# Performance work log

Hardware: AMD Instinct MI355X
Metric: run time of the kernel (lower is better)

## Reference

```python
import jax, jax.numpy as jnp
import numpy as np

B, C, N = 8, 512, 4096
G = 8          # GroupNorm groups (8 <= C)
EPS = 1e-6


def setup_inputs() -> dict:
    key = jax.random.key(0)
    ks = jax.random.split(key, 5)
    return {
        "x": jax.random.normal(ks[0], (B, C, N), dtype=jnp.float32),
        "qkv_w": jax.random.normal(ks[1], (3 * C, C), dtype=jnp.float32) * (C ** -0.5),
        "qkv_b": jax.random.normal(ks[2], (3 * C,), dtype=jnp.float32) * 0.02,
        "proj_w": jax.random.normal(ks[3], (C, C), dtype=jnp.float32) * (C ** -0.5),
        "proj_b": jax.random.normal(ks[4], (C,), dtype=jnp.float32) * 0.02,
        "gn_scale": jnp.ones((C,), dtype=jnp.float32),
        "gn_bias": jnp.zeros((C,), dtype=jnp.float32),
    }


def group_norm(x, scale, bias):
    b, c, n = x.shape
    xr = x.reshape(b, G, c // G, n)
    mean = xr.mean(axis=(2, 3), keepdims=True)
    var = xr.var(axis=(2, 3), keepdims=True)
    h = ((xr - mean) * jax.lax.rsqrt(var + EPS)).reshape(b, c, n)
    return h * scale[None, :, None] + bias[None, :, None]


def reference(x, qkv_w, qkv_b, proj_w, proj_b, gn_scale, gn_bias):
    c = x.shape[1]
    h = group_norm(x, gn_scale, gn_bias)
    # 1x1 Conv1d == channel-mixing GEMM
    qkv = jnp.einsum('oc,bcn->bon', qkv_w, h) + qkv_b[None, :, None]
    q, k, v = jnp.split(qkv, 3, axis=1)           # each [B, C, N]
    q = q * (c ** -0.5)
    k = jax.nn.softmax(k, axis=-1)                # softmax over tokens
    # linear attention: context = k v^T over tokens, then project q
    context = jnp.einsum('bdn,ben->bde', k, v)    # [B, C, C]
    out = jnp.einsum('bde,bdn->ben', context, q)  # [B, C, N]
    y = jnp.einsum('oc,bcn->bon', proj_w, out) + proj_b[None, :, None]
    return x + y
```

## Files before the change

kernel.cpp:

```cpp
#include <hip/hip_runtime.h>

#define BB 8
#define CC 512
#define NT 4096
#define GG 8
#define CPG 64
#define EPSF 1e-6f
#define SQK 0.04419417382415922f

typedef __attribute__((ext_vector_type(8))) short bf16x8;
typedef __attribute__((ext_vector_type(4))) float f32x4;

#define OFF_RED  0
#define OFF_PB2  4096
#define OFF_IZ   270336
#define OFF_WKV  274432
#define OFF_PWB  536576
#define OFF_WQT  667648
#define OFF_MB   798720
#define OFF_PBF  1847296
#define OFF_CTXB 2895872
#define OFF_PCTX 3944448
#define OFF_HT   12333056
#define OFF_KVB  20721664

__device__ __forceinline__ ushort f2bf(float f) {
  union { float f; uint u; } v; v.f = f;
  uint r = (v.u + 0x7fffu + ((v.u >> 16) & 1u)) >> 16;
  return (ushort)r;
}
__device__ __forceinline__ float bf2f(ushort h) {
  union { uint u; float f; } v; v.u = ((uint)h) << 16;
  return v.f;
}
__device__ __forceinline__ uint pk(float a, float b) {
  return (uint)f2bf(a) | ((uint)f2bf(b) << 16);
}
__device__ __forceinline__ void gload16(const ushort* g, ushort* l) {
  __builtin_amdgcn_global_load_lds((const __attribute__((address_space(1))) void*)g,
                                   (__attribute__((address_space(3))) void*)l, 16, 0, 0);
}
#define KSWZ(kofs, row) ((kofs) ^ ((((row) >> 1) & 3) << 3))

__global__ __launch_bounds__(256) void gn_stats1(const float* __restrict__ x,
                                                 float* __restrict__ red) {
  int bg = blockIdx.y, chunk = blockIdx.x;
  const float4* p4 = (const float4*)(x + (size_t)bg * (CPG * NT) + (size_t)chunk * 32768);
  int tid = threadIdx.x;
  float s = 0.f, sq = 0.f;
  for (int i = tid; i < 8192; i += 256) {
    float4 v = p4[i];
    s  += v.x + v.y + v.z + v.w;
    sq += v.x * v.x + v.y * v.y + v.z * v.z + v.w * v.w;
  }
  for (int off = 32; off > 0; off >>= 1) {
    s  += __shfl_down(s, off);
    sq += __shfl_down(sq, off);
  }
  __shared__ float ls[4], lq[4];
  int wid = tid >> 6, lane = tid & 63;
  if (lane == 0) { ls[wid] = s; lq[wid] = sq; }
  __syncthreads();
  if (tid == 0) {
    red[(bg * 8 + chunk) * 2]     = ls[0] + ls[1] + ls[2] + ls[3];
    red[(bg * 8 + chunk) * 2 + 1] = lq[0] + lq[1] + lq[2] + lq[3];
  }
}

__global__ __launch_bounds__(256) void wconv2(const float* __restrict__ qkv_w,
                                              const float* __restrict__ proj_w,
                                              ushort* __restrict__ wkvb,
                                              ushort* __restrict__ pwb) {
  int bid = blockIdx.x;
  if (bid < 512) {
    int idx = (bid * 256 + threadIdx.x) * 4;
    float4 v = *(const float4*)(qkv_w + (size_t)CC * CC + idx);
    *(uint2*)(wkvb + idx) = make_uint2(pk(v.x, v.y), pk(v.z, v.w));
  } else {
    int idx = ((bid - 512) * 256 + threadIdx.x) * 4;
    float4 v = *(const float4*)(proj_w + idx);
    *(uint2*)(pwb + idx) = make_uint2(pk(v.x, v.y), pk(v.z, v.w));
  }
}

__global__ __launch_bounds__(256) void wqt_kernel(const float* __restrict__ qkv_w,
                                                  ushort* __restrict__ wqT) {
  __shared__ float t[32][33];
  int d0 = blockIdx.y * 32, c0 = blockIdx.x * 32;
  int tid = threadIdx.x;
  int r = tid >> 3, c4 = (tid & 7) * 4;
  float4 v = *(const float4*)(qkv_w + (size_t)(d0 + r) * CC + c0 + c4);
  t[r][c4] = v.x; t[r][c4 + 1] = v.y; t[r][c4 + 2] = v.z; t[r][c4 + 3] = v.w;
  __syncthreads();
  int r2 = tid >> 3, d4 = (tid & 7) * 4;
  uint w0 = pk(t[d4][r2], t[d4 + 1][r2]);
  uint w1 = pk(t[d4 + 2][r2], t[d4 + 3][r2]);
  *(uint2*)&wqT[(size_t)(c0 + r2) * CC + d0 + d4] = make_uint2(w0, w1);
}

__global__ __launch_bounds__(256) void ht_kernel(
    const float* __restrict__ x, const float* __restrict__ red,
    const float* __restrict__ gn_scale, const float* __restrict__ gn_bias,
    ushort* __restrict__ hT) {
  __shared__ float ts[64][68];
  __shared__ float la[64], lb[64];
  int b = blockIdx.z, g = blockIdx.y, n0 = blockIdx.x * 64;
  int c0 = g * 64;
  int tid = threadIdx.x;
  if (tid == 0) {
    int bg = b * 8 + g;
    float s = 0.f, sq = 0.f;
#pragma unroll
    for (int i = 0; i < 8; i++) {
      s  += red[(bg * 8 + i) * 2];
      sq += red[(bg * 8 + i) * 2 + 1];
    }
    float mean = s / (float)(CPG * NT);
    float var  = sq / (float)(CPG * NT) - mean * mean;
    ts[0][0] = mean; ts[0][1] = rsqrtf(var + EPSF);
  }
  __syncthreads();
  if (tid < 64) {
    float mean = ts[0][0], rstd = ts[0][1];
    float a = gn_scale[c0 + tid] * rstd;
    la[tid] = a;
    lb[tid] = gn_bias[c0 + tid] - mean * a;
  }
  __syncthreads();
  int tn = (tid & 15) * 4, tc = tid >> 4;
#pragma unroll
  for (int it = 0; it < 4; it++) {
    int c = tc + it * 16;
    float a  = la[c];
    float bb = lb[c];
    float4 v = *(const float4*)(x + ((size_t)(b * CC + c0 + c)) * NT + n0 + tn);
    ts[c][tn]     = a * v.x + bb;
    ts[c][tn + 1] = a * v.y + bb;
    ts[c][tn + 2] = a * v.z + bb;
    ts[c][tn + 3] = a * v.w + bb;
  }
  __syncthreads();
#pragma unroll
  for (int it = 0; it < 2; it++) {
    int idx = tid + it * 256;
    int n = idx >> 3, c8 = (idx & 7) * 8;
    uint w[4];
#pragma unroll
    for (int j = 0; j < 4; j++)
      w[j] = pk(ts[c8 + 2 * j][n], ts[c8 + 2 * j + 1][n]);
    *(uint4*)&hT[((size_t)b * NT + n0 + n) * CC + c0 + c8] = make_uint4(w[0], w[1], w[2], w[3]);
  }
}

#define TBUF 16384

__device__ __forceinline__ void stage256(const ushort* __restrict__ G, ushort* L,
                                         int LD, int wave, int lane) {
  int rw = wave * 8 + (lane >> 3);
  int cg = lane & 7;
#pragma unroll
  for (int s = 0; s < 4; s++) {
    int row = s * 64 + rw;
    int gcol = (cg ^ (row & 7)) * 8;
    gload16(G + (size_t)row * LD + gcol, L + s * 4096 + wave * 512);
  }
}

template <int NTILES>
__device__ __forceinline__ void mfma256c(const ushort* __restrict__ A,
                                         const ushort* __restrict__ B,
                                         int LDA, int LDB, ushort* As, ushort* Bs,
                                         int tid, f32x4 acc[8][4]) {
  int wave = tid >> 6, lane = tid & 63;
  int wr = wave >> 2, wc = wave & 3;
  stage256(A, As, LDA, wave, lane);
  stage256(B, Bs, LDB, wave, lane);
  const ushort* gA = A + 64;
  const ushort* gB = B + 64;
  int rowA = wr * 128 + (lane & 15);
  int rowB = wc * 64 + (lane & 15);
  int kg0 = lane >> 4;
#pragma unroll 1
  for (int t = 0; t < NTILES; t++) {
    __builtin_amdgcn_s_barrier();
    asm volatile("" ::: "memory");
    if (t + 1 < NTILES) {
      stage256(gA, As + ((t + 1) & 1) * TBUF, LDA, wave, lane);
      stage256(gB, Bs + ((t + 1) & 1) * TBUF, LDB, wave, lane);
      gA += 64; gB += 64;
      asm volatile("s_waitcnt vmcnt(8)" ::: "memory");
    } else {
      asm volatile("s_waitcnt vmcnt(0)" ::: "memory");
    }
    __builtin_amdgcn_s_barrier();
    asm volatile("" ::: "memory");
    const ushort* Ab = As + (t & 1) * TBUF;
    const ushort* Bb = Bs + (t & 1) * TBUF;
#pragma unroll
    for (int kk = 0; kk < 2; kk++) {
      int kg = kg0 + kk * 4;
      bf16x8 bfr[4];
#pragma unroll
      for (int ni = 0; ni < 4; ni++) {
        int r = rowB + ni * 16;
        bfr[ni] = *(const bf16x8*)(Bb + r * 64 + ((kg ^ (r & 7)) << 3));
      }
#pragma unroll
      for (int mi = 0; mi < 8; mi++) {
        int r = rowA + mi * 16;
        bf16x8 afr = *(const bf16x8*)(Ab + r * 64 + ((kg ^ (r & 7)) << 3));
#pragma unroll
        for (int ni = 0; ni < 4; ni++)
          acc[mi][ni] = __builtin_amdgcn_mfma_f32_16x16x32_bf16(afr, bfr[ni], acc[mi][ni], 0, 0, 0);
      }
    }
  }
}

#define DBUF 8192

__device__ __forceinline__ void stage32(const ushort* __restrict__ G, ushort* L,
                                        int LD, int tid) {
#pragma unroll
  for (int s = 0; s < 2; s++) {
    int row = s * 128 + (tid >> 2);
    int gcol = ((tid & 3) ^ (row & 3)) * 8;
    gload16(G + (size_t)row * LD + gcol, L + s * 4096 + (tid >> 6) * 512);
  }
}

template <int NT32>
__device__ __forceinline__ void mfma256d(const ushort* __restrict__ A,
                                         const ushort* __restrict__ B,
                                         int LDA, int LDB, ushort* As, ushort* Bs,
                                         int tid, f32x4 acc[8][4]) {
  int wave = tid >> 6, lane = tid & 63;
  int wr = wave >> 2, wc = wave & 3;
#pragma unroll
  for (int t0 = 0; t0 < 2; t0++) {
    stage32(A + t0 * 32, As + t0 * DBUF, LDA, tid);
    stage32(B + t0 * 32, Bs + t0 * DBUF, LDB, tid);
  }
  const ushort* gA = A + 64;
  const ushort* gB = B + 64;
  int rowA = wr * 128 + (lane & 15);
  int rowB = wc * 64 + (lane & 15);
  int kg = lane >> 4;
#pragma unroll 1
  for (int t = 0; t < NT32; t++) {
    if (t + 2 < NT32) {
      stage32(gA, As + ((t + 2) & 3) * DBUF, LDA, tid);
      stage32(gB, Bs + ((t + 2) & 3) * DBUF, LDB, tid);
      gA += 32; gB += 32;
      asm volatile("s_waitcnt vmcnt(8)" ::: "memory");
    } else if (t + 1 < NT32) {
      asm volatile("s_waitcnt vmcnt(4)" ::: "memory");
    } else {
      asm volatile("s_waitcnt vmcnt(0)" ::: "memory");
    }
    __builtin_amdgcn_s_barrier();
    asm volatile("" ::: "memory");
    const ushort* Ab = As + (t & 3) * DBUF;
    const ushort* Bb = Bs + (t & 3) * DBUF;
    bf16x8 bfr[4];
#pragma unroll
    for (int ni = 0; ni < 4; ni++) {
      int r = rowB + ni * 16;
      bfr[ni] = *(const bf16x8*)(Bb + r * 32 + (((kg) ^ (r & 3)) << 3));
    }
#pragma unroll
    for (int mi = 0; mi < 8; mi++) {
      int r = rowA + mi * 16;
      bf16x8 afr = *(const bf16x8*)(Ab + r * 32 + (((kg) ^ (r & 3)) << 3));
#pragma unroll
      for (int ni = 0; ni < 4; ni++)
        acc[mi][ni] = __builtin_amdgcn_mfma_f32_16x16x32_bf16(afr, bfr[ni], acc[mi][ni], 0, 0, 0);
    }
    asm volatile("" ::: "memory");
    __builtin_amdgcn_s_barrier();
    asm volatile("" ::: "memory");
  }
}

template <int KTOT, int LDA, int LDB>
__device__ __forceinline__ void mfma_loop64(const ushort* __restrict__ A,
                                            const ushort* __restrict__ B,
                                            ushort* As, ushort* Bs, int tid,
                                            f32x4 acc[2][2]) {
  int wave = tid >> 6, lane = tid & 63;
  int srow = tid >> 2;
  int kofs = KSWZ((tid & 3) * 8, srow & 15);
  const ushort* ga = A + (size_t)srow * LDA + kofs;
  const ushort* gb = B + (size_t)srow * LDB + kofs;
  int lo = wave * 512;
  int wm = (wave >> 1) * 32, wn = (wave & 1) * 32;
  int rowl = lane & 15;
  int kread = KSWZ((lane >> 4) * 8, rowl);
  int aoff = (wm + rowl) * 32 + kread;
  int boff = (wn + rowl) * 32 + kread;
  constexpr int NIT = KTOT / 32;
  gload16(ga, As + lo); gload16(gb, Bs + lo);
  ga += 32; gb += 32;
#pragma unroll 1
  for (int t = 0; t < NIT; t++) {
    int cb = (t & 1) * 2048;
    int nb = 2048 - cb;
    if (t + 1 < NIT) {
      gload16(ga, As + nb + lo); gload16(gb, Bs + nb + lo);
      ga += 32; gb += 32;
      asm volatile("s_waitcnt vmcnt(2)" ::: "memory");
    } else {
      asm volatile("s_waitcnt vmcnt(0)" ::: "memory");
    }
    __builtin_amdgcn_s_barrier();
    asm volatile("" ::: "memory");
    bf16x8 a[2], b[2];
#pragma unroll
    for (int m = 0; m < 2; m++) a[m] = *(const bf16x8*)(As + cb + aoff + m * 512);
#pragma unroll
    for (int n = 0; n < 2; n++) b[n] = *(const bf16x8*)(Bs + cb + boff + n * 512);
#pragma unroll
    for (int m = 0; m < 2; m++)
#pragma unroll
      for (int n = 0; n < 2; n++)
        acc[m][n] = __builtin_amdgcn_mfma_f32_16x16x32_bf16(a[m], b[n], acc[m][n], 0, 0, 0);
    asm volatile("" ::: "memory");
    __builtin_amdgcn_s_barrier();
    asm volatile("" ::: "memory");
  }
}

__global__ __launch_bounds__(512) void kv_gemm_bf16(
    const ushort* __restrict__ wkvb, const ushort* __restrict__ hT,
    const float* __restrict__ qkv_b, ushort* __restrict__ kvb) {
  extern __shared__ ushort lds[];
  ushort* As = lds;
  ushort* Bs = lds + 4 * DBUF;
  int b = blockIdx.z, n0 = blockIdx.x * 256, m0 = blockIdx.y * 256;
  int tid = threadIdx.x;
  f32x4 acc[8][4] = {{{0.f, 0.f, 0.f, 0.f}}};
  mfma256d<16>(wkvb + (size_t)m0 * CC, hT + (size_t)b * NT * CC + (size_t)n0 * CC,
               CC, CC, As, Bs, tid, acc);
  int wave = tid >> 6, lane = tid & 63;
  int wr = wave >> 2, wc = wave & 3;
  int col = lane & 15, rb = (lane >> 4) * 4;
  bool isK = (m0 < 512);
#pragma unroll
  for (int mi = 0; mi < 8; mi++)
#pragma unroll
    for (int j = 0; j < 4; j++) {
      int gm = m0 + wr * 128 + mi * 16 + rb + j;
      float bias = qkv_b[CC + gm];
      ushort* orow = kvb + ((size_t)(b * 1024 + gm)) * NT + n0 + wc * 64 + col;
#pragma unroll
      for (int ni = 0; ni < 4; ni++) {
        float val = acc[mi][ni][j] + bias;
        if (isK) val = __expf(val);
        orow[ni * 16] = f2bf(val);
      }
    }
}

__global__ __launch_bounds__(256) void zred(const ushort* __restrict__ kvb,
                                            float* __restrict__ invZ) {
  int row = blockIdx.x;
  int b = row >> 9, d = row & 511;
  const ushort* p = kvb + ((size_t)(b * 1024 + d)) * NT;
  int tid = threadIdx.x;
  uint4 r0 = *(const uint4*)(p + tid * 16);
  uint4 r1 = *(const uint4*)(p + tid * 16 + 8);
  uint w[8] = {r0.x, r0.y, r0.z, r0.w, r1.x, r1.y, r1.z, r1.w};
  float s = 0.f;
#pragma unroll
  for (int i = 0; i < 8; i++) {
    union { uint u; float f; } lo, hi;
    lo.u = w[i] << 16; hi.u = w[i] & 0xffff0000u;
    s += lo.f + hi.f;
  }
  for (int off = 32; off > 0; off >>= 1) s += __shfl_down(s, off);
  __shared__ float red[4];
  int wid = tid >> 6, lane = tid & 63;
  if (lane == 0) red[wid] = s;
  __syncthreads();
  if (tid == 0) invZ[row] = 1.f / (red[0] + red[1] + red[2] + red[3]);
}

__global__ __launch_bounds__(512) void ctx_gemm_split(
    const ushort* __restrict__ kvb, ushort* __restrict__ pctx) {
  extern __shared__ ushort lds[];
  ushort* As = lds;
  ushort* Bs = lds + 2 * TBUF;
  int e0 = blockIdx.x * 256, d0 = blockIdx.y * 256;
  int bz = blockIdx.z, b = bz >> 3, s = bz & 7;
  int tid = threadIdx.x;
  f32x4 acc[8][4] = {{{0.f, 0.f, 0.f, 0.f}}};
  const ushort* K = kvb + (size_t)b * 1024 * NT + (size_t)d0 * NT + s * 512;
  const ushort* V = kvb + ((size_t)b * 1024 + 512) * NT + (size_t)e0 * NT + s * 512;
  mfma256c<8>(K, V, NT, NT, As, Bs, tid, acc);
  int wave = tid >> 6, lane = tid & 63;
  int wr = wave >> 2, wc = wave & 3;
  int col = lane & 15, rb = (lane >> 4) * 4;
#pragma unroll
  for (int mi = 0; mi < 8; mi++)
#pragma unroll
    for (int j = 0; j < 4; j++) {
      int gd = d0 + wr * 128 + mi * 16 + rb + j;
      ushort* orow = pctx + ((size_t)(b * 8 + s) * CC + gd) * CC + e0 + wc * 64 + col;
#pragma unroll
      for (int ni = 0; ni < 4; ni++)
        orow[ni * 16] = f2bf(acc[mi][ni][j]);
    }
}

__global__ __launch_bounds__(256) void ctx_red(const ushort* __restrict__ pctx,
                                               const float* __restrict__ invZ,
                                               ushort* __restrict__ ctxb) {
  int t = blockIdx.x * 256 + threadIdx.x;
  int b = t >> 15;
  int r = (t & 32767) * 8;
  int d = r >> 9;
  float iz = invZ[b * 512 + d];
  const ushort* base = pctx + (size_t)b * 8 * 262144 + r;
  float f[8] = {};
#pragma unroll
  for (int s = 0; s < 8; s++) {
    uint4 v = *(const uint4*)(base + (size_t)s * 262144);
    uint w[4] = {v.x, v.y, v.z, v.w};
#pragma unroll
    for (int j = 0; j < 4; j++) {
      union { uint u; float f; } lo, hi;
      lo.u = w[j] << 16; hi.u = w[j] & 0xffff0000u;
      f[2 * j] += lo.f; f[2 * j + 1] += hi.f;
    }
  }
  uint o[4];
#pragma unroll
  for (int j = 0; j < 4; j++) o[j] = pk(f[2 * j] * iz, f[2 * j + 1] * iz);
  *(uint4*)(ctxb + (size_t)b * 262144 + r) = make_uint4(o[0], o[1], o[2], o[3]);
}

__global__ __launch_bounds__(256) void m_gemm_bf16(
    const ushort* __restrict__ pwb, const ushort* __restrict__ ctxb,
    ushort* __restrict__ Mb) {
  __shared__ ushort As[4096], Bs[4096];
  int b = blockIdx.z, d0 = blockIdx.x * 64, o0 = blockIdx.y * 64;
  int tid = threadIdx.x;
  f32x4 acc[2][2] = {{{0.f, 0.f, 0.f, 0.f}}};
  mfma_loop64<CC, CC, CC>(pwb + (size_t)o0 * CC,
                          ctxb + (size_t)b * CC * CC + (size_t)d0 * CC, As, Bs, tid, acc);
  int wave = tid >> 6, lane = tid & 63;
  int wm = (wave >> 1) * 32, wn = (wave & 1) * 32;
  int col = lane & 15, rb = (lane >> 4) * 4;
#pragma unroll
  for (int m = 0; m < 2; m++)
#pragma unroll
    for (int n = 0; n < 2; n++)
#pragma unroll
      for (int j = 0; j < 4; j++) {
        int go = o0 + wm + m * 16 + rb + j;
        int gd = d0 + wn + n * 16 + col;
        Mb[((size_t)b * CC + go) * CC + gd] = f2bf(acc[m][n][j] * SQK);
      }
}

__global__ __launch_bounds__(256) void p_gemm_bf16(
    const ushort* __restrict__ Mb, const ushort* __restrict__ wqT,
    ushort* __restrict__ Pb) {
  __shared__ ushort As[4096], Bs[4096];
  int b = blockIdx.z, c0 = blockIdx.x * 64, o0 = blockIdx.y * 64;
  int tid = threadIdx.x;
  f32x4 acc[2][2] = {{{0.f, 0.f, 0.f, 0.f}}};
  mfma_loop64<CC, CC, CC>(Mb + (size_t)b * CC * CC + (size_t)o0 * CC,
                          wqT + (size_t)c0 * CC, As, Bs, tid, acc);
  int wave = tid >> 6, lane = tid & 63;
  int wm = (wave >> 1) * 32, wn = (wave & 1) * 32;
  int col = lane & 15, rb = (lane >> 4) * 4;
#pragma unroll
  for (int m = 0; m < 2; m++)
#pragma unroll
    for (int n = 0; n < 2; n++)
#pragma unroll
      for (int j = 0; j < 4; j++) {
        int go = o0 + wm + m * 16 + rb + j;
        int gc = c0 + wn + n * 16 + col;
        Pb[((size_t)b * CC + go) * CC + gc] = f2bf(acc[m][n][j]);
      }
}

__global__ __launch_bounds__(256) void pb2_kernel(
    const ushort* __restrict__ Mb, const float* __restrict__ qkv_b,
    const float* __restrict__ proj_b, float* __restrict__ pb2) {
  int b = blockIdx.x, og = blockIdx.y;
  int r = og * 64 + (threadIdx.x >> 2);
  int q = threadIdx.x & 3;
  const ushort* Mr = Mb + ((size_t)(b * CC + r)) * CC + q * 128;
  const float* bq = qkv_b + q * 128;
  float s = 0.f;
#pragma unroll
  for (int i = 0; i < 16; i++) {
    uint4 v = *(const uint4*)(Mr + i * 8);
    uint w[4] = {v.x, v.y, v.z, v.w};
#pragma unroll
    for (int j = 0; j < 4; j++) {
      union { uint u; float f; } lo, hi;
      lo.u = w[j] << 16; hi.u = w[j] & 0xffff0000u;
      s += lo.f * bq[i * 8 + 2 * j] + hi.f * bq[i * 8 + 2 * j + 1];
    }
  }
  s += __shfl_xor(s, 1);
  s += __shfl_xor(s, 2);
  if (q == 0) pb2[b * CC + r] = s + proj_b[r];
}

__global__ __launch_bounds__(512) void final_gemm_bf16(
    const float* __restrict__ x, const ushort* __restrict__ Pb,
    const ushort* __restrict__ hT, const float* __restrict__ pb2,
    float* __restrict__ out) {
  extern __shared__ ushort lds[];
  ushort* As = lds;
  ushort* Bs = lds + 2 * TBUF;
  int b = blockIdx.z, n0 = blockIdx.x * 256, m0 = blockIdx.y * 256;
  int tid = threadIdx.x;
  f32x4 acc[8][4] = {{{0.f, 0.f, 0.f, 0.f}}};
  mfma256c<8>(Pb + (size_t)b * CC * CC + (size_t)m0 * CC,
              hT + (size_t)b * NT * CC + (size_t)n0 * CC, CC, CC, As, Bs, tid, acc);
  int wave = tid >> 6, lane = tid & 63;
  int wr = wave >> 2, wc = wave & 3;
  int col = lane & 15, rb = (lane >> 4) * 4;
#pragma unroll
  for (int mi = 0; mi < 8; mi++)
#pragma unroll
    for (int j = 0; j < 4; j++) {
      int gm = m0 + wr * 128 + mi * 16 + rb + j;
      float bias = pb2[b * CC + gm];
      size_t rowoff = ((size_t)(b * CC + gm)) * NT + n0 + wc * 64 + col;
#pragma unroll
      for (int ni = 0; ni < 4; ni++)
        out[rowoff + ni * 16] = acc[mi][ni][j] + bias + x[rowoff + ni * 16];
    }
}

extern "C" void kernel_launch(void* const* d_in, const int* in_sizes, int n_in,
                              void* d_out, int out_size, void* d_ws, size_t ws_size,
                              hipStream_t stream) {
  const float* x        = (const float*)d_in[0];
  const float* qkv_w    = (const float*)d_in[1];
  const float* qkv_b    = (const float*)d_in[2];
  const float* proj_w   = (const float*)d_in[3];
  const float* proj_b   = (const float*)d_in[4];
  const float* gn_scale = (const float*)d_in[5];
  const float* gn_bias  = (const float*)d_in[6];
  float* out = (float*)d_out;
  float* ws  = (float*)d_ws;

  float*  red   = ws + OFF_RED;
  float*  pb2   = ws + OFF_PB2;
  float*  invZ  = ws + OFF_IZ;
  ushort* wkvb  = (ushort*)(ws + OFF_WKV);
  ushort* pwb   = (ushort*)(ws + OFF_PWB);
  ushort* wqT   = (ushort*)(ws + OFF_WQT);
  ushort* Mb    = (ushort*)(ws + OFF_MB);
  ushort* Pb    = (ushort*)(ws + OFF_PBF);
  ushort* ctxb  = (ushort*)(ws + OFF_CTXB);
  ushort* pctx  = (ushort*)(ws + OFF_PCTX);
  ushort* hT    = (ushort*)(ws + OFF_HT);
  ushort* kvb   = (ushort*)(ws + OFF_KVB);

  constexpr int DSM = 4 * TBUF * 2;
  hipFuncSetAttribute((const void*)kv_gemm_bf16,
                      hipFuncAttributeMaxDynamicSharedMemorySize, DSM);
  hipFuncSetAttribute((const void*)ctx_gemm_split,
                      hipFuncAttributeMaxDynamicSharedMemorySize, DSM);
  hipFuncSetAttribute((const void*)final_gemm_bf16,
                      hipFuncAttributeMaxDynamicSharedMemorySize, DSM);

  gn_stats1<<<dim3(8, 64), 256, 0, stream>>>(x, red);
  wconv2<<<768, 256, 0, stream>>>(qkv_w, proj_w, wkvb, pwb);
  wqt_kernel<<<dim3(16, 16), 256, 0, stream>>>(qkv_w, wqT);
  ht_kernel<<<dim3(64, 8, 8), 256, 0, stream>>>(x, red, gn_scale, gn_bias, hT);
  kv_gemm_bf16<<<dim3(16, 4, 8), 512, DSM, stream>>>(wkvb, hT, qkv_b, kvb);
  zred<<<4096, 256, 0, stream>>>(kvb, invZ);
  ctx_gemm_split<<<dim3(2, 2, 64), 512, DSM, stream>>>(kvb, pctx);
  ctx_red<<<1024, 256, 0, stream>>>(pctx, invZ, ctxb);
  m_gemm_bf16<<<dim3(8, 8, 8), 256, 0, stream>>>(pwb, ctxb, Mb);
  p_gemm_bf16<<<dim3(8, 8, 8), 256, 0, stream>>>(Mb, wqT, Pb);
  pb2_kernel<<<dim3(8, 8), 256, 0, stream>>>(Mb, qkv_b, proj_b, pb2);
  final_gemm_bf16<<<dim3(16, 2, 8), 512, DSM, stream>>>(x, Pb, hT, pb2, out);
}
```

Baseline: 190.0 us.

## Use 128x128 tiles for final GEMM and revert kv GEMM to mfma256c

The final projection GEMM moves from 256x256 tiles to a new 128x128-tile routine with 64-wide K stages and double buffering. The grid grows from 256 to 1024 blocks, which gives better CU occupancy and more blocks in flight for the memory-heavy epilogue that reads x and writes out. The kv GEMM switches from the 4-stage mfma256d pipeline back to the mfma256c routine, and mfma256d is removed. Smaller tiles lower operand reuse per block, and dropping the deeper prefetch in kv_gemm may expose load latency there.

```diff
diff --git a/kernel.cpp b/kernel.cpp
--- a/kernel.cpp
+++ b/kernel.cpp
@@ -217,68 +217,64 @@
   }
 }
 
-#define DBUF 8192
-
-__device__ __forceinline__ void stage32(const ushort* __restrict__ G, ushort* L,
-                                        int LD, int tid) {
+__device__ __forceinline__ void stage128(const ushort* __restrict__ G, ushort* L,
+                                         int LD, int tid) {
 #pragma unroll
   for (int s = 0; s < 2; s++) {
-    int row = s * 128 + (tid >> 2);
-    int gcol = ((tid & 3) ^ (row & 3)) * 8;
+    int row = s * 64 + (tid >> 3);
+    int gcol = ((tid & 7) ^ (row & 7)) * 8;
     gload16(G + (size_t)row * LD + gcol, L + s * 4096 + (tid >> 6) * 512);
   }
 }
 
-template <int NT32>
-__device__ __forceinline__ void mfma256d(const ushort* __restrict__ A,
-                                         const ushort* __restrict__ B,
-                                         int LDA, int LDB, ushort* As, ushort* Bs,
-                                         int tid, f32x4 acc[8][4]) {
+template <int NTILES>
+__device__ __forceinline__ void mfma128(const ushort* __restrict__ A,
+                                        const ushort* __restrict__ B,
+                                        int LDA, int LDB, ushort* As, ushort* Bs,
+                                        int tid, f32x4 acc[4][2]) {
   int wave = tid >> 6, lane = tid & 63;
   int wr = wave >> 2, wc = wave & 3;
-#pragma unroll
-  for (int t0 = 0; t0 < 2; t0++) {
-    stage32(A + t0 * 32, As + t0 * DBUF, LDA, tid);
-    stage32(B + t0 * 32, Bs + t0 * DBUF, LDB, tid);
-  }
+  stage128(A, As, LDA, tid);
+  stage128(B, Bs, LDB, tid);
   const ushort* gA = A + 64;
   const ushort* gB = B + 64;
-  int rowA = wr * 128 + (lane & 15);
-  int rowB = wc * 64 + (lane & 15);
-  int kg = lane >> 4;
+  int rowA = wr * 64 + (lane & 15);
+  int rowB = wc * 32 + (lane & 15);
+  int kg0 = lane >> 4;
 #pragma unroll 1
-  for (int t = 0; t < NT32; t++) {
-    if (t + 2 < NT32) {
-      stage32(gA, As + ((t + 2) & 3) * DBUF, LDA, tid);
-      stage32(gB, Bs + ((t + 2) & 3) * DBUF, LDB, tid);
-      gA += 32; gB += 32;
-      asm volatile("s_waitcnt vmcnt(8)" ::: "memory");
-    } else if (t + 1 < NT32) {
+  for (int t = 0; t < NTILES; t++) {
+    __builtin_amdgcn_s_barrier();
+    asm volatile("" ::: "memory");
+    if (t + 1 < NTILES) {
+      stage128(gA, As + ((t + 1) & 1) * 8192, LDA, tid);
+      stage128(gB, Bs + ((t + 1) & 1) * 8192, LDB, tid);
+      gA += 64; gB += 64;
       asm volatile("s_waitcnt vmcnt(4)" ::: "memory");
     } else {
       asm volatile("s_waitcnt vmcnt(0)" ::: "memory");
     }
     __builtin_amdgcn_s_barrier();
     asm volatile("" ::: "memory");
-    const ushort* Ab = As + (t & 3) * DBUF;
-    const ushort* Bb = Bs + (t & 3) * DBUF;
-    bf16x8 bfr[4];
-#pragma unroll
-    for (int ni = 0; ni < 4; ni++) {
-      int r = rowB + ni * 16;
-      bfr[ni] = *(const bf16x8*)(Bb + r * 32 + (((kg) ^ (r & 3)) << 3));
-    }
-#pragma unroll
-    for (int mi = 0; mi < 8; mi++) {
-      int r = rowA + mi * 16;
-      bf16x8 afr = *(const bf16x8*)(Ab + r * 32 + (((kg) ^ (r & 3)) << 3));
-#pragma unroll
-      for (int ni = 0; ni < 4; ni++)
-        acc[mi][ni] = __builtin_amdgcn_mfma_f32_16x16x32_bf16(afr, bfr[ni], acc[mi][ni], 0, 0, 0);
-    }
-    asm volatile("" ::: "memory");
-    __builtin_amdgcn_s_barrier();
-    asm volatile("" ::: "memory");
+    const ushort* Ab = As + (t & 1) * 8192;
+    const ushort* Bb = Bs + (t & 1) * 8192;
+#pragma unroll
+    for (int kk = 0; kk < 2; kk++) {
+      int kg = kg0 + kk * 4;
+      bf16x8 bfr[2];
+#pragma unroll
+      for (int ni = 0; ni < 2; ni++) {
+        int r = rowB + ni * 16;
+        bfr[ni] = *(const bf16x8*)(Bb + r * 64 + ((kg ^ (r & 7)) << 3));
+      }
+#pragma unroll
+      for (int mi = 0; mi < 4; mi++) {
+        int r = rowA + mi * 16;
+        bf16x8 afr = *(const bf16x8*)(Ab + r * 64 + ((kg ^ (r & 7)) << 3));
+#pragma unroll
+        for (int ni = 0; ni < 2; ni++)
+          acc[mi][ni] = __builtin_amdgcn_mfma_f32_16x16x32_bf16(afr, bfr[ni], acc[mi][ni], 0, 0, 0);
+      }
+    }
   }
 }
 
@@ -335,12 +331,12 @@
     const float* __restrict__ qkv_b, ushort* __restrict__ kvb) {
   extern __shared__ ushort lds[];
   ushort* As = lds;
-  ushort* Bs = lds + 4 * DBUF;
+  ushort* Bs = lds + 2 * TBUF;
   int b = blockIdx.z, n0 = blockIdx.x * 256, m0 = blockIdx.y * 256;
   int tid = threadIdx.x;
   f32x4 acc[8][4] = {{{0.f, 0.f, 0.f, 0.f}}};
-  mfma256d<16>(wkvb + (size_t)m0 * CC, hT + (size_t)b * NT * CC + (size_t)n0 * CC,
-               CC, CC, As, Bs, tid, acc);
+  mfma256c<8>(wkvb + (size_t)m0 * CC, hT + (size_t)b * NT * CC + (size_t)n0 * CC,
+              CC, CC, As, Bs, tid, acc);
   int wave = tid >> 6, lane = tid & 63;
   int wr = wave >> 2, wc = wave & 3;
   int col = lane & 15, rb = (lane >> 4) * 4;
@@ -518,24 +514,24 @@
     float* __restrict__ out) {
   extern __shared__ ushort lds[];
   ushort* As = lds;
-  ushort* Bs = lds + 2 * TBUF;
-  int b = blockIdx.z, n0 = blockIdx.x * 256, m0 = blockIdx.y * 256;
-  int tid = threadIdx.x;
-  f32x4 acc[8][4] = {{{0.f, 0.f, 0.f, 0.f}}};
-  mfma256c<8>(Pb + (size_t)b * CC * CC + (size_t)m0 * CC,
-              hT + (size_t)b * NT * CC + (size_t)n0 * CC, CC, CC, As, Bs, tid, acc);
+  ushort* Bs = lds + 2 * 8192;
+  int b = blockIdx.z, n0 = blockIdx.x * 128, m0 = blockIdx.y * 128;
+  int tid = threadIdx.x;
+  f32x4 acc[4][2] = {{{0.f, 0.f, 0.f, 0.f}}};
+  mfma128<8>(Pb + (size_t)b * CC * CC + (size_t)m0 * CC,
+             hT + (size_t)b * NT * CC + (size_t)n0 * CC, CC, CC, As, Bs, tid, acc);
   int wave = tid >> 6, lane = tid & 63;
   int wr = wave >> 2, wc = wave & 3;
   int col = lane & 15, rb = (lane >> 4) * 4;
 #pragma unroll
-  for (int mi = 0; mi < 8; mi++)
+  for (int mi = 0; mi < 4; mi++)
 #pragma unroll
     for (int j = 0; j < 4; j++) {
-      int gm = m0 + wr * 128 + mi * 16 + rb + j;
+      int gm = m0 + wr * 64 + mi * 16 + rb + j;
       float bias = pb2[b * CC + gm];
-      size_t rowoff = ((size_t)(b * CC + gm)) * NT + n0 + wc * 64 + col;
-#pragma unroll
-      for (int ni = 0; ni < 4; ni++)
+      size_t rowoff = ((size_t)(b * CC + gm)) * NT + n0 + wc * 32 + col;
+#pragma unroll
+      for (int ni = 0; ni < 2; ni++)
         out[rowoff + ni * 16] = acc[mi][ni][j] + bias + x[rowoff + ni * 16];
     }
 }
@@ -566,13 +562,14 @@
   ushort* hT    = (ushort*)(ws + OFF_HT);
   ushort* kvb   = (ushort*)(ws + OFF_KVB);
 
-  constexpr int DSM = 4 * TBUF * 2;
+  constexpr int DSM  = 4 * TBUF * 2;
+  constexpr int DSM2 = 4 * 8192 * 2;
   hipFuncSetAttribute((const void*)kv_gemm_bf16,
                       hipFuncAttributeMaxDynamicSharedMemorySize, DSM);
   hipFuncSetAttribute((const void*)ctx_gemm_split,
                       hipFuncAttributeMaxDynamicSharedMemorySize, DSM);
   hipFuncSetAttribute((const void*)final_gemm_bf16,
-                      hipFuncAttributeMaxDynamicSharedMemorySize, DSM);
+                      hipFuncAttributeMaxDynamicSharedMemorySize, DSM2);
 
   gn_stats1<<<dim3(8, 64), 256, 0, stream>>>(x, red);
   wconv2<<<768, 256, 0, stream>>>(qkv_w, proj_w, wkvb, pwb);
@@ -585,5 +582,5 @@
   m_gemm_bf16<<<dim3(8, 8, 8), 256, 0, stream>>>(pwb, ctxb, Mb);
   p_gemm_bf16<<<dim3(8, 8, 8), 256, 0, stream>>>(Mb, wqT, Pb);
   pb2_kernel<<<dim3(8, 8), 256, 0, stream>>>(Mb, qkv_b, proj_b, pb2);
-  final_gemm_bf16<<<dim3(16, 2, 8), 512, DSM, stream>>>(x, Pb, hT, pb2, out);
-}
+  final_gemm_bf16<<<dim3(32, 4, 8), 512, DSM2, stream>>>(x, Pb, hT, pb2, out);
+}
```

After: 184.0 us. 1.03x faster.
